# Kernel optimization log

Hardware: AMD Instinct MI355X
Metric: run time of the kernel (lower is better)

## Reference

```python
import jax, jax.numpy as jnp
import numpy as np

N1 = 4097
N2 = 8192


def setup_inputs() -> dict:
    key = jax.random.key(0)
    kx, ka, kb, km = jax.random.split(key, 4)
    x = jax.random.normal(kx, ((N1 - 1) * N2 + 1,), dtype=jnp.float32)
    a = jax.random.uniform(ka, (1,), dtype=jnp.float32)
    b = jax.random.uniform(kb, (N2, N1 - 1), dtype=jnp.float32)
    mu = jax.random.uniform(km, (1,), dtype=jnp.float32)
    return {"x": x, "a": a, "b": b, "mu": mu}


def reference(x, a, b, mu):
    n2, n1m1 = b.shape  # (n2, n1-1)
    n1 = n1m1 + 1
    # y = x[1 : (n1-1)*n2 + 1].reshape(n2, n1-1)
    y = x[1:(n1 - 1) * n2 + 1].reshape(n2, n1 - 1)
    # Original loop: i in range(n1-2), j in range(n2-1); term uses y[j, i-1],
    # which at i=0 wraps to the LAST column (negative indexing). Reproduce via roll.
    y_cur = y[: n2 - 1, : n1 - 2]                       # y[j, i]
    y_prev = jnp.roll(y, 1, axis=1)[: n2 - 1, : n1 - 2]  # y[j, i-1] with wraparound
    terms = b[: n2 - 1, : n1 - 2] * (y_cur - y_prev ** 2) ** 2
    return -a * (x[0] - mu) ** 2 - jnp.sum(terms)
```

## Files before the change

### kernel.cpp

```cpp
#include <hip/hip_runtime.h>


#define ROWS   8191u
#define GRID   2048
#define BLOCK  256
#define ROWSPB 4u

__global__ __launch_bounds__(BLOCK) void rosen_partial(
    const float* __restrict__ x, const float* __restrict__ b,
    float* __restrict__ partial)
{
    const unsigned lane = threadIdx.x & 63u;
    const unsigned w    = threadIdx.x >> 6;
    float acc = 0.0f;

    #pragma unroll 1
    for (unsigned k = 0; k < ROWSPB; ++k) {
        const unsigned r = blockIdx.x * ROWSPB + k;
        if (r >= ROWS) break;
        const size_t rowoff = (size_t)r * 4096u;
        const size_t base   = rowoff + w * 1024u + lane * 4u;

        float4 xv0 = *(const float4*)(x + base);
        float4 xv1 = *(const float4*)(x + base + 256);
        float4 xv2 = *(const float4*)(x + base + 512);
        float4 xv3 = *(const float4*)(x + base + 768);
        float4 bv0 = *(const float4*)(b + base);
        float4 bv1 = *(const float4*)(b + base + 256);
        float4 bv2 = *(const float4*)(b + base + 512);
        float4 bv3 = *(const float4*)(b + base + 768);

        float tail = x[rowoff + w * 1024u + 1024u];
        float wrapv = 0.0f;
        if (threadIdx.x == 0) wrapv = x[rowoff + 4096u];
        if (threadIdx.x == BLOCK - 1) bv3.w = 0.0f;

        float n0 = __shfl_down(xv0.x, 1, 64);
        float n1 = __shfl_down(xv1.x, 1, 64);
        float n2 = __shfl_down(xv2.x, 1, 64);
        float n3 = __shfl_down(xv3.x, 1, 64);
        float c1 = __shfl(xv1.x, 0, 64);
        float c2 = __shfl(xv2.x, 0, 64);
        float c3 = __shfl(xv3.x, 0, 64);
        if (lane == 63u) { n0 = c1; n1 = c2; n2 = c3; n3 = tail; }

        float pv = xv0.x;
        if (threadIdx.x == 0) pv = wrapv;

        float d;
        d = xv0.y - pv    * pv;     acc += bv0.x * d * d;
        d = xv0.z - xv0.y * xv0.y;  acc += bv0.y * d * d;
        d = xv0.w - xv0.z * xv0.z;  acc += bv0.z * d * d;
        d = n0    - xv0.w * xv0.w;  acc += bv0.w * d * d;
        d = xv1.y - xv1.x * xv1.x;  acc += bv1.x * d * d;
        d = xv1.z - xv1.y * xv1.y;  acc += bv1.y * d * d;
        d = xv1.w - xv1.z * xv1.z;  acc += bv1.z * d * d;
        d = n1    - xv1.w * xv1.w;  acc += bv1.w * d * d;
        d = xv2.y - xv2.x * xv2.x;  acc += bv2.x * d * d;
        d = xv2.z - xv2.y * xv2.y;  acc += bv2.y * d * d;
        d = xv2.w - xv2.z * xv2.z;  acc += bv2.z * d * d;
        d = n2    - xv2.w * xv2.w;  acc += bv2.w * d * d;
        d = xv3.y - xv3.x * xv3.x;  acc += bv3.x * d * d;
        d = xv3.z - xv3.y * xv3.y;  acc += bv3.y * d * d;
        d = xv3.w - xv3.z * xv3.z;  acc += bv3.z * d * d;
        d = n3    - xv3.w * xv3.w;  acc += bv3.w * d * d;
    }

    #pragma unroll
    for (int off = 32; off > 0; off >>= 1)
        acc += __shfl_down(acc, off, 64);

    __shared__ float sred[4];
    if (lane == 0) sred[w] = acc;
    __syncthreads();
    if (threadIdx.x == 0)
        partial[blockIdx.x] = sred[0] + sred[1] + sred[2] + sred[3];
}

__global__ __launch_bounds__(256) void rosen_final(const float* __restrict__ partial,
                                                   const float* __restrict__ x,
                                                   const float* __restrict__ a,
                                                   const float* __restrict__ mu,
                                                   float* __restrict__ out)
{
    float acc = 0.0f;
    for (int i = threadIdx.x; i < GRID; i += 256)
        acc += partial[i];

    #pragma unroll
    for (int off = 32; off > 0; off >>= 1)
        acc += __shfl_down(acc, off, 64);

    __shared__ float sred[4];
    const int lane = threadIdx.x & 63;
    const int wid  = threadIdx.x >> 6;
    if (lane == 0) sred[wid] = acc;
    __syncthreads();
    if (threadIdx.x == 0) {
        float total = sred[0] + sred[1] + sred[2] + sred[3];
        float dd = x[0] - mu[0];
        out[0] = -a[0] * dd * dd - total;
    }
}

extern "C" void kernel_launch(void* const* d_in, const int* in_sizes, int n_in,
                              void* d_out, int out_size, void* d_ws, size_t ws_size,
                              hipStream_t stream) {
    const float* x  = (const float*)d_in[0];
    const float* a  = (const float*)d_in[1];
    const float* b  = (const float*)d_in[2];
    const float* mu = (const float*)d_in[3];
    float* out     = (float*)d_out;
    float* partial = (float*)d_ws;

    rosen_partial<<<GRID, BLOCK, 0, stream>>>(x, b, partial);
    rosen_final<<<1, 256, 0, stream>>>(partial, x, a, mu, out);
}
```

Measured before the change: 283.2 us.

## Double-buffer rows through LDS via direct global_load_lds with 16 rows per block

Rows of x and b are now staged into LDS with the global_load_lds builtin, double-buffered so the next row's loads are issued while the current row is computed. Each block handles 16 rows instead of 4 on a grid of 512 blocks. Neighbour and wrap values are read from LDS instead of through extra global loads. The cost is 64 KB of LDS per block and two barriers per row, which cuts occupancy and adds sync overhead. The vmcnt-based waits also rely on exact counts of outstanding loads.

```diff
diff --git a/kernel.cpp b/kernel.cpp
--- a/kernel.cpp
+++ b/kernel.cpp
@@ -1,69 +1,76 @@
 #include <hip/hip_runtime.h>
 
 
-#define ROWS   8191u
-#define GRID   2048
+#define ROWS   8191
+#define GRID   512
 #define BLOCK  256
-#define ROWSPB 4u
+#define RPB    16
+
+#define GLDS4(gp, lp)  __builtin_amdgcn_global_load_lds(                     \
+    (const __attribute__((address_space(1))) void*)(gp),                     \
+    (__attribute__((address_space(3))) void*)(lp), 4, 0, 0)
+#define GLDS16(gp, lp) __builtin_amdgcn_global_load_lds(                     \
+    (const __attribute__((address_space(1))) void*)(gp),                     \
+    (__attribute__((address_space(3))) void*)(lp), 16, 0, 0)
 
 __global__ __launch_bounds__(BLOCK) void rosen_partial(
     const float* __restrict__ x, const float* __restrict__ b,
     float* __restrict__ partial)
 {
-    const unsigned lane = threadIdx.x & 63u;
-    const unsigned w    = threadIdx.x >> 6;
+    __shared__ float sx[2][4096];
+    __shared__ float sb[2][4096];
+
+    const unsigned t    = threadIdx.x;
+    const unsigned lane = t & 63u;
+    const unsigned w    = t >> 6;
+    const unsigned row0 = blockIdx.x * RPB;
+    const int nrows     = (row0 + RPB <= ROWS) ? RPB : (int)(ROWS - row0);
+
+    auto stage = [&](int rr, int buf) {
+        const size_t rowbase = (size_t)(row0 + rr) * 4096u;
+        const float* xs = x + rowbase + 1 + w * 1024u + lane;
+        float*       xd = &sx[buf][w * 1024u];
+        #pragma unroll
+        for (int j = 0; j < 16; ++j)
+            GLDS4(xs + j * 64, xd + j * 64);
+        const float* bs = b + rowbase + w * 1024u + lane * 4u;
+        float*       bd = &sb[buf][w * 1024u];
+        #pragma unroll
+        for (int j = 0; j < 4; ++j)
+            GLDS16(bs + j * 256, bd + j * 256);
+    };
+
     float acc = 0.0f;
+    stage(0, 0);
 
-    #pragma unroll 1
-    for (unsigned k = 0; k < ROWSPB; ++k) {
-        const unsigned r = blockIdx.x * ROWSPB + k;
-        if (r >= ROWS) break;
-        const size_t rowoff = (size_t)r * 4096u;
-        const size_t base   = rowoff + w * 1024u + lane * 4u;
+    for (int rr = 0; rr < nrows; ++rr) {
+        const int cur = rr & 1;
+        if (rr + 1 < nrows) {
+            stage(rr + 1, cur ^ 1);
+            asm volatile("s_waitcnt vmcnt(20)" ::: "memory");
+        } else {
+            asm volatile("s_waitcnt vmcnt(0)" ::: "memory");
+        }
+        __builtin_amdgcn_s_barrier();
 
-        float4 xv0 = *(const float4*)(x + base);
-        float4 xv1 = *(const float4*)(x + base + 256);
-        float4 xv2 = *(const float4*)(x + base + 512);
-        float4 xv3 = *(const float4*)(x + base + 768);
-        float4 bv0 = *(const float4*)(b + base);
-        float4 bv1 = *(const float4*)(b + base + 256);
-        float4 bv2 = *(const float4*)(b + base + 512);
-        float4 bv3 = *(const float4*)(b + base + 768);
-
-        float tail = x[rowoff + w * 1024u + 1024u];
-        float wrapv = 0.0f;
-        if (threadIdx.x == 0) wrapv = x[rowoff + 4096u];
-        if (threadIdx.x == BLOCK - 1) bv3.w = 0.0f;
-
-        float n0 = __shfl_down(xv0.x, 1, 64);
-        float n1 = __shfl_down(xv1.x, 1, 64);
-        float n2 = __shfl_down(xv2.x, 1, 64);
-        float n3 = __shfl_down(xv3.x, 1, 64);
-        float c1 = __shfl(xv1.x, 0, 64);
-        float c2 = __shfl(xv2.x, 0, 64);
-        float c3 = __shfl(xv3.x, 0, 64);
-        if (lane == 63u) { n0 = c1; n1 = c2; n2 = c3; n3 = tail; }
-
-        float pv = xv0.x;
-        if (threadIdx.x == 0) pv = wrapv;
-
-        float d;
-        d = xv0.y - pv    * pv;     acc += bv0.x * d * d;
-        d = xv0.z - xv0.y * xv0.y;  acc += bv0.y * d * d;
-        d = xv0.w - xv0.z * xv0.z;  acc += bv0.z * d * d;
-        d = n0    - xv0.w * xv0.w;  acc += bv0.w * d * d;
-        d = xv1.y - xv1.x * xv1.x;  acc += bv1.x * d * d;
-        d = xv1.z - xv1.y * xv1.y;  acc += bv1.y * d * d;
-        d = xv1.w - xv1.z * xv1.z;  acc += bv1.z * d * d;
-        d = n1    - xv1.w * xv1.w;  acc += bv1.w * d * d;
-        d = xv2.y - xv2.x * xv2.x;  acc += bv2.x * d * d;
-        d = xv2.z - xv2.y * xv2.y;  acc += bv2.y * d * d;
-        d = xv2.w - xv2.z * xv2.z;  acc += bv2.z * d * d;
-        d = n2    - xv2.w * xv2.w;  acc += bv2.w * d * d;
-        d = xv3.y - xv3.x * xv3.x;  acc += bv3.x * d * d;
-        d = xv3.z - xv3.y * xv3.y;  acc += bv3.y * d * d;
-        d = xv3.w - xv3.z * xv3.z;  acc += bv3.z * d * d;
-        d = n3    - xv3.w * xv3.w;  acc += bv3.w * d * d;
+        const float* xt = sx[cur];
+        const float* bt = sb[cur];
+        #pragma unroll
+        for (int k = 0; k < 4; ++k) {
+            const unsigned cb = w * 1024u + k * 256u;
+            float4 v  = *(const float4*)(xt + cb + 4u * lane);
+            float4 bv = *(const float4*)(bt + cb + 4u * lane);
+            float  pu = xt[(cb - 1u) & 4095u];
+            float  p  = __shfl_up(v.w, 1, 64);
+            if (lane == 0) p = pu;
+            if (t == BLOCK - 1 && k == 3) bv.w = 0.0f;
+            float d;
+            d = v.x - p   * p;    acc += bv.x * d * d;
+            d = v.y - v.x * v.x;  acc += bv.y * d * d;
+            d = v.z - v.y * v.y;  acc += bv.z * d * d;
+            d = v.w - v.z * v.z;  acc += bv.w * d * d;
+        }
+        __builtin_amdgcn_s_barrier();
     }
 
     #pragma unroll
@@ -73,7 +80,7 @@
     __shared__ float sred[4];
     if (lane == 0) sred[w] = acc;
     __syncthreads();
-    if (threadIdx.x == 0)
+    if (t == 0)
         partial[blockIdx.x] = sred[0] + sred[1] + sred[2] + sred[3];
 }
 
```

After: 281.7 us. Within noise of the previous version (-0.5%).
